# Optimization experiments

Measured on AMD Instinct MI355X. Metric: run time of the kernel, lower is better.

The kernel has to match this reference:

```python
import jax, jax.numpy as jnp
import numpy as np

D = 8        # q_ndim (= dof_ndim)
HID = 200    # hidden_size
N = 16384    # batch of states
EPS = 0.1    # qdot regularizer coefficient in L()


def _lagrangian(z, Ws, bs):
    # z: (2D,) = [q, qdot]; angular_dims=() so CosSin is an identity pass-through
    v = z[D:]
    h = z
    for W, b in zip(Ws[:-1], bs[:-1]):
        h = jax.nn.softplus(h @ W + b)   # FCsoftplus blocks
    L = (h @ Ws[-1] + bs[-1])[0]          # final Linear -> scalar (Reshape(-1))
    return L + EPS * jnp.dot(v, v)


def setup_inputs():
    key = jax.random.key(0)
    ks = jax.random.split(key, 5)
    z = jax.random.normal(ks[0], (N, 2 * D), dtype=jnp.float32)
    t = jnp.zeros((), dtype=jnp.float32)

    def lin(k, fi, fo, scale):
        return (jax.random.normal(k, (fi, fo), dtype=jnp.float32)
                * jnp.float32(scale / np.sqrt(fi)))

    W0 = lin(ks[1], 2 * D, HID, 1.0)
    W1 = lin(ks[2], HID, HID, 1.0)
    W2 = lin(ks[3], HID, HID, 1.0)
    W3 = lin(ks[4], HID, 1, 0.01)  # small head keeps mass matrix M well conditioned
    b0 = jnp.zeros((HID,), jnp.float32)  # zero_bias init per FCsoftplus/Linear
    b1 = jnp.zeros((HID,), jnp.float32)
    b2 = jnp.zeros((HID,), jnp.float32)
    b3 = jnp.zeros((1,), jnp.float32)
    return dict(t=t, z=z, W0=W0, b0=b0, W1=W1, b1=b1, W2=W2, b2=b2, W3=W3, b3=b3)


def reference(t, z, W0, b0, W1, b1, W2, b2, W3, b3):
    # Euler-Lagrange dynamics (LagrangianDynamics):
    #   M a = dL/dq - (d2L/dq dv) v,  M = d2L/dv2;  dz/dt = [v, a]
    Ws = (W0, W1, W2, W3)
    bs = (b0, b1, b2, b3)
    Lfn = lambda zz: _lagrangian(zz, Ws, bs)

    def dyn_single(zi):
        g = jax.grad(Lfn)(zi)              # (2D,)  = [dL/dq, dL/dv]
        H = jax.jacfwd(jax.grad(Lfn))(zi)  # (2D,2D) Hessian of L wrt z
        v = zi[D:]
        M = H[D:, D:]                      # d(dL/dv)/dv  -> mass matrix
        C = H[D:, :D]                      # d(dL/dv)/dq
        F = g[:D] - C @ v
        a = jnp.linalg.solve(M, F)
        return jnp.concatenate([v, a])     # (2D,)

    return jax.vmap(dyn_single)(z)         # (N, 2D)
```

## Files before the change

kernel.cpp:

```cpp
#include <hip/hip_runtime.h>
#include <math.h>

#define DD 8
#define ZD 16
#define HID 200
#define EPSL 0.1f
#define BS 16
#define NTHREADS 1024
#define NKC 7
#define NMT 13
#define XSTR 216
#define CSTR 216
#define WSTR 208
#define HSTR 20
#define NT4 4

#define KSC 1024.0f
#define SSC 64.0f
#define INV_K (1.0f/1024.0f)
#define INV_KS (1.0f/65536.0f)

typedef _Float16 half8 __attribute__((ext_vector_type(8)));
typedef _Float16 half4v __attribute__((ext_vector_type(4)));
typedef _Float16 half2v __attribute__((ext_vector_type(2)));
typedef float float4v __attribute__((ext_vector_type(4)));

#define S4 (NKC*NMT*64*8)
#define OFF_W1T 0
#define OFF_W2T (S4)
#define OFF_W1  (2*S4)
#define OFF_W2  (3*S4)
#define OFF_W0T (4*S4)
#define OFF_W0  (4*S4 + NMT*64*8)
#define WS_HALFS (4*S4 + NMT*64*8 + NKC*64*8)

#define CFSZ  (16*CSTR)
#define O_XT  0
#define O_XB  (128*XSTR + 8)
#define O_CF  (O_XB + 128*XSTR)
#define O_BSH (O_CF + 5*CFSZ)
#define O_W0T (O_BSH + 4*WSTR)
#define O_XZ  (O_W0T + 8*WSTR + 24)
#define O_GSH (O_XZ + 16*40)
#define O_HR  (O_GSH + 256)
#define SMEM_HALFS (O_HR + 128*HSTR*2)

__global__ void prep(const float* __restrict__ W0, const float* __restrict__ W1,
                     const float* __restrict__ W2, _Float16* __restrict__ ws)
{
    int idx = blockIdx.x * 256 + threadIdx.x;
    if (idx >= WS_HALFS) return;
    float v = 0.f;
    if (idx < 4*S4) {
        int arr = idx / S4, e = idx % S4;
        int kc = e / (NMT*64*8); int r = e % (NMT*64*8);
        int mt = r / (64*8); r %= 64*8;
        int lane = r / 8, j = r % 8;
        int m = mt*16 + (lane & 15);
        int k = kc*32 + (lane >> 4)*8 + j;
        if (m < HID && k < HID) {
            if      (arr == 0) v = W1[k*HID + m];
            else if (arr == 1) v = W2[k*HID + m];
            else if (arr == 2) v = W1[m*HID + k];
            else               v = W2[m*HID + k];
        }
    } else if (idx < OFF_W0) {
        int e = idx - OFF_W0T;
        int mt = e / (64*8); int r = e % (64*8);
        int lane = r / 8, j = r % 8;
        int m = mt*16 + (lane & 15);
        int k = (lane >> 4)*8 + j;
        if (m < HID && k < ZD) v = W0[k*HID + m];
    } else {
        int e = idx - OFF_W0;
        int kc = e / (64*8); int r = e % (64*8);
        int lane = r / 8, j = r % 8;
        int m = (lane & 15);
        int k = kc*32 + (lane >> 4)*8 + j;
        if (k < HID) v = W0[m*HID + k];
    }
    ws[idx] = (_Float16)v;
}

__device__ __forceinline__ half4v pk4(float4v a) {
    half2v lo = __builtin_bit_cast(half2v, __builtin_amdgcn_cvt_pkrtz(a.x, a.y));
    half2v hi = __builtin_bit_cast(half2v, __builtin_amdgcn_cvt_pkrtz(a.z, a.w));
    return __builtin_shufflevector(lo, hi, 0, 1, 2, 3);
}
__device__ __forceinline__ void sig_sp(float x, float& sp, float& sg) {
    float e = __expf(-fabsf(x));
    float r = 1.0f / (1.0f + e);
    sg = (x >= 0.f) ? r : (1.0f - r);
    sp = fmaxf(x, 0.f) + __logf(1.f + e);
}

template<int NTILES>
__device__ __forceinline__ void run_mv(const half8* __restrict__ Asw,
                                       const _Float16* __restrict__ Xsrc,
                                       int mt0, int mtc, int lane,
                                       float4v acc[2][NTILES])
{
    const int lm = lane & 15, q = lane >> 4;
#pragma unroll
    for (int m = 0; m < 2; ++m)
#pragma unroll
        for (int n = 0; n < NTILES; ++n)
            acc[m][n] = (float4v){0.f, 0.f, 0.f, 0.f};
    for (int kc = 0; kc < NKC; ++kc) {
        half8 a[2];
#pragma unroll
        for (int m = 0; m < 2; ++m)
            if (m < mtc) a[m] = Asw[(kc*NMT + mt0 + m)*64 + lane];
        half8 x[NTILES];
#pragma unroll
        for (int n = 0; n < NTILES; ++n)
            x[n] = *(const half8*)(Xsrc + (n*16 + lm)*XSTR + kc*32 + q*8);
#pragma unroll
        for (int m = 0; m < 2; ++m)
            if (m < mtc)
#pragma unroll
                for (int n = 0; n < NTILES; ++n)
                    acc[m][n] = __builtin_amdgcn_mfma_f32_16x16x32_f16(a[m], x[n], acc[m][n], 0, 0, 0);
    }
}

__global__ void __launch_bounds__(NTHREADS, 4)
lnn_main(const float* __restrict__ z,
         const float* __restrict__ W0, const float* __restrict__ b0,
         const float* __restrict__ b1, const float* __restrict__ b2,
         const float* __restrict__ W3,
         const _Float16* __restrict__ ws,
         float* __restrict__ out)
{
    __shared__ alignas(16) _Float16 smem[SMEM_HALFS];
    _Float16* const Xt  = smem + O_XT;
    _Float16* const Xb  = smem + O_XB;
    _Float16* const Cf  = smem + O_CF;
    _Float16* const bsh = smem + O_BSH;
    _Float16* const w0t = smem + O_W0T;
    _Float16* const Xz  = smem + O_XZ;
    float*    const gsh = (float*)(smem + O_GSH);
    float*    const Hr  = (float*)(smem + O_HR);
    _Float16* const FB  = smem + O_HR;

    const int tid  = threadIdx.x;
    const int wave = tid >> 6;
    const int lane = tid & 63;
    const int lm   = lane & 15;
    const int q    = lane >> 4;
    const int s0   = blockIdx.x * BS;

    const int twm  = wave >> 1;
    const int twn  = wave & 1;
    const int mt0t = (twm < 5) ? twm*2 : (twm + 5);
    const int mtct = (twm < 5) ? 2 : 1;

    const half8* W1Tsw = (const half8*)(ws + OFF_W1T);
    const half8* W2Tsw = (const half8*)(ws + OFF_W2T);
    const half8* W1sw  = (const half8*)(ws + OFF_W1);
    const half8* W2sw  = (const half8*)(ws + OFF_W2);
    const half8* W0Tsw = (const half8*)(ws + OFF_W0T);
    const half8* W0sw  = (const half8*)(ws + OFF_W0);

    if (tid < 256) {
        int s = tid >> 4, k = tid & 15;
        Xz[s*40 + k]      = (_Float16)z[(s0 + s)*ZD + k];
        Xz[s*40 + 16 + k] = (_Float16)0.f;
    }
    for (int idx = tid; idx < 128*16; idx += NTHREADS) {
        int r = idx >> 4, c = 200 + (idx & 15);
        Xt[r*XSTR + c] = (_Float16)0.f;
        Xb[r*XSTR + c] = (_Float16)0.f;
    }
    for (int idx = tid; idx < 16*16; idx += NTHREADS) {
        int r = idx >> 4, c = 200 + (idx & 15);
        FB[r*XSTR + c] = (_Float16)0.f;
    }
    if (tid < 8) {
        Xt[128*XSTR + tid] = (_Float16)0.f;
        FB[16*XSTR + tid]  = (_Float16)0.f;
    }
    for (int idx = tid; idx < 5*16*8; idx += NTHREADS) {
        int j = idx >> 7, r = (idx >> 3) & 15, c = 208 + (idx & 7);
        Cf[j*CFSZ + r*CSTR + c] = (_Float16)0.f;
    }
    for (int idx = tid; idx < 4*WSTR; idx += NTHREADS) {
        int l = idx / WSTR, u = idx % WSTR;
        float v = 0.f;
        if (u < HID) {
            if      (l == 0) v = b0[u];
            else if (l == 1) v = b1[u];
            else if (l == 2) v = b2[u];
            else             v = KSC * W3[u];
        }
        bsh[idx] = (_Float16)v;
    }
    for (int idx = tid; idx < 8*WSTR + 24; idx += NTHREADS) {
        int t = idx / WSTR, u = idx % WSTR;
        w0t[idx] = (_Float16)((t < 8 && u < HID) ? SSC * W0[(DD + t)*HID + u] : 0.f);
    }
    __syncthreads();

    float4v acc1[2][1];
    float4v acc4[2][NT4];
    const int ubf = wave*16 + q*4;

    if (wave < NMT) {
        acc1[0][0] = (float4v){0.f,0.f,0.f,0.f};
        half8 xz = *(const half8*)(Xz + lm*40 + q*8);
        half8 aw = W0Tsw[wave*64 + lane];
        acc1[0][0] = __builtin_amdgcn_mfma_f32_16x16x32_f16(aw, xz, acc1[0][0], 0, 0, 0);
        half4v bb = *(const half4v*)(&bsh[0*WSTR + ubf]);
        float h[4], p[4];
#pragma unroll
        for (int r = 0; r < 4; ++r) {
            float av = acc1[0][0][r] + (float)bb[r];
            sig_sp(av, h[r], p[r]);
        }
        *(half4v*)(&FB[lm*XSTR + ubf])          = pk4((float4v){h[0],h[1],h[2],h[3]});
        *(half4v*)(&Cf[0*CFSZ + lm*CSTR + ubf]) = pk4((float4v){p[0],p[1],p[2],p[3]});
    }
    __syncthreads();

    if (wave < NMT) run_mv<1>(W1Tsw, FB, wave, 1, lane, acc1);
    __syncthreads();
    if (wave < NMT) {
        half4v bb = *(const half4v*)(&bsh[1*WSTR + ubf]);
        float h[4], p[4];
#pragma unroll
        for (int r = 0; r < 4; ++r) {
            float av = acc1[0][0][r] + (float)bb[r];
            sig_sp(av, h[r], p[r]);
        }
        *(half4v*)(&FB[lm*XSTR + ubf])          = pk4((float4v){h[0],h[1],h[2],h[3]});
        *(half4v*)(&Cf[1*CFSZ + lm*CSTR + ubf]) = pk4((float4v){p[0],p[1],p[2],p[3]});
    }
    __syncthreads();

    {
#pragma unroll
        for (int m = 0; m < 2; ++m)
#pragma unroll
            for (int n = 0; n < NT4; ++n)
                acc4[m][n] = (float4v){0.f, 0.f, 0.f, 0.f};
        for (int kc = 0; kc < NKC; ++kc) {
            half8 a[2];
#pragma unroll
            for (int m = 0; m < 2; ++m)
                if (m < mtct) a[m] = W1Tsw[(kc*NMT + mt0t + m)*64 + lane];
            half8 p0 = *(const half8*)(Cf + 0*CFSZ + lm*CSTR + kc*32 + q*8);
            half8 x[NT4];
#pragma unroll
            for (int n = 0; n < NT4; ++n) {
                half8 w0 = *(const half8*)(w0t + (twn*NT4 + n)*WSTR + kc*32 + q*8);
                x[n] = p0 * w0;
            }
#pragma unroll
            for (int m = 0; m < 2; ++m)
                if (m < mtct)
#pragma unroll
                    for (int n = 0; n < NT4; ++n)
                        acc4[m][n] = __builtin_amdgcn_mfma_f32_16x16x32_f16(a[m], x[n], acc4[m][n], 0, 0, 0);
        }
        if (wave < NMT) run_mv<1>(W2Tsw, FB, wave, 1, lane, acc1);
    }
    __syncthreads();
#pragma unroll
    for (int m = 0; m < 2; ++m)
        if (m < mtct) {
            const int ub = (mt0t + m)*16 + q*4;
            half4v p1 = *(const half4v*)(&Cf[1*CFSZ + lm*CSTR + ub]);
#pragma unroll
            for (int n = 0; n < NT4; ++n) {
                int row = (twn*NT4 + n)*16 + lm;
                *(half4v*)(&Xt[row*XSTR + ub]) = pk4(acc4[m][n]) * p1;
            }
        }
    if (wave < NMT) {
        half4v bb = *(const half4v*)(&bsh[2*WSTR + ubf]);
        half4v w3 = *(const half4v*)(&bsh[3*WSTR + ubf]);
        float d2[4], c2[4];
#pragma unroll
        for (int r = 0; r < 4; ++r) {
            float av = acc1[0][0][r] + (float)bb[r];
            float e = __expf(-fabsf(av));
            float rr = 1.f / (1.f + e);
            float sg = (av >= 0.f) ? rr : (1.f - rr);
            float wk = (float)w3[r];
            d2[r] = wk * sg;
            c2[r] = wk * sg * (1.f - sg);
        }
        *(half4v*)(&FB[lm*XSTR + ubf])          = pk4((float4v){d2[0],d2[1],d2[2],d2[3]});
        *(half4v*)(&Cf[2*CFSZ + lm*CSTR + ubf]) = pk4((float4v){c2[0],c2[1],c2[2],c2[3]});
    }
    __syncthreads();

    run_mv<NT4>(W2Tsw, Xt + twn*64*XSTR, mt0t, mtct, lane, acc4);
    if (wave < NMT) run_mv<1>(W2sw, FB, wave, 1, lane, acc1);
    __syncthreads();
#pragma unroll
    for (int m = 0; m < 2; ++m)
        if (m < mtct) {
            const int ub = (mt0t + m)*16 + q*4;
            half4v c2 = *(const half4v*)(&Cf[2*CFSZ + lm*CSTR + ub]);
#pragma unroll
            for (int n = 0; n < NT4; ++n) {
                int row = (twn*NT4 + n)*16 + lm;
                *(half4v*)(&Xb[row*XSTR + ub]) = pk4(acc4[m][n]) * c2;
            }
        }
    if (wave < NMT) {
        half4v p1 = *(const half4v*)(&Cf[1*CFSZ + lm*CSTR + ubf]);
        half4v u1 = pk4(acc1[0][0]);
        half4v one = {(_Float16)1.f,(_Float16)1.f,(_Float16)1.f,(_Float16)1.f};
        *(half4v*)(&FB[lm*XSTR + ubf])          = u1 * p1;
        *(half4v*)(&Cf[3*CFSZ + lm*CSTR + ubf]) = u1 * (one - p1);
    }
    __syncthreads();

    run_mv<NT4>(W2sw, Xb + twn*64*XSTR, mt0t, mtct, lane, acc4);
    if (wave < NMT) run_mv<1>(W1sw, FB, wave, 1, lane, acc1);
    __syncthreads();
#pragma unroll
    for (int m = 0; m < 2; ++m)
        if (m < mtct) {
            const int ub = (mt0t + m)*16 + q*4;
            half4v p1 = *(const half4v*)(&Cf[1*CFSZ + lm*CSTR + ub]);
            half4v c3 = *(const half4v*)(&Cf[3*CFSZ + lm*CSTR + ub]);
#pragma unroll
            for (int n = 0; n < NT4; ++n) {
                int row = (twn*NT4 + n)*16 + lm;
                half4v th1 = *(const half4v*)(&Xt[row*XSTR + ub]);
                *(half4v*)(&Xb[row*XSTR + ub]) = pk4(acc4[m][n]) * p1 + c3 * th1;
            }
        }
    if (wave < NMT) {
        half4v p0 = *(const half4v*)(&Cf[0*CFSZ + lm*CSTR + ubf]);
        half4v u0 = pk4(acc1[0][0]);
        half4v one = {(_Float16)1.f,(_Float16)1.f,(_Float16)1.f,(_Float16)1.f};
        half4v d0 = u0 * p0;
        *(half4v*)(&FB[lm*XSTR + ubf])          = d0;
        *(half4v*)(&Cf[4*CFSZ + lm*CSTR + ubf]) = d0 * (one - p0);
    }
    __syncthreads();

    run_mv<NT4>(W1sw, Xb + twn*64*XSTR, mt0t, mtct, lane, acc4);
    if (wave == 13) {
        float4v g = (float4v){0.f,0.f,0.f,0.f};
        for (int kc = 0; kc < NKC; ++kc) {
            half8 a = W0sw[kc*64 + lane];
            half8 x = *(const half8*)(FB + lm*XSTR + kc*32 + q*8);
            g = __builtin_amdgcn_mfma_f32_16x16x32_f16(a, x, g, 0, 0, 0);
        }
        if (q < 2) {
            float4v gv;
            gv.x = g.x*INV_K; gv.y = g.y*INV_K; gv.z = g.z*INV_K; gv.w = g.w*INV_K;
            *(float4v*)(&gsh[lm*8 + q*4]) = gv;
        }
    }
#pragma unroll
    for (int m = 0; m < 2; ++m)
        if (m < mtct) {
            const int ub = (mt0t + m)*16 + q*4;
            half4v p0 = *(const half4v*)(&Cf[0*CFSZ + lm*CSTR + ub]);
            half4v c4 = *(const half4v*)(&Cf[4*CFSZ + lm*CSTR + ub]);
#pragma unroll
            for (int n = 0; n < NT4; ++n) {
                int row = (twn*NT4 + n)*16 + lm;
                half4v w0 = *(const half4v*)(&w0t[(twn*NT4 + n)*WSTR + ub]);
                *(half4v*)(&Xt[row*XSTR + ub]) = pk4(acc4[m][n]) * p0 + c4 * w0;
            }
        }
    __syncthreads();

    if (wave < 8) {
        float4v hacc = (float4v){0.f,0.f,0.f,0.f};
        for (int kc = 0; kc < NKC; ++kc) {
            half8 a = W0sw[kc*64 + lane];
            half8 x = *(const half8*)(Xt + (wave*16 + lm)*XSTR + kc*32 + q*8);
            hacc = __builtin_amdgcn_mfma_f32_16x16x32_f16(a, x, hacc, 0, 0, 0);
        }
        int row = wave*16 + lm;
        float4v hv;
        hv.x = hacc.x*INV_KS; hv.y = hacc.y*INV_KS;
        hv.z = hacc.z*INV_KS; hv.w = hacc.w*INV_KS;
        *(float4v*)(&Hr[row*HSTR + q*4]) = hv;
    }
    __syncthreads();

    if (tid < BS) {
        const int s = tid;
        float M[DD][DD], F[DD], v[DD], a[DD];
#pragma unroll
        for (int c = 0; c < DD; ++c) v[c] = z[(s0 + s)*ZD + DD + c];
#pragma unroll
        for (int r = 0; r < DD; ++r) {
            float f = gsh[s*8 + r];
#pragma unroll
            for (int c = 0; c < DD; ++c) {
                M[r][c] = Hr[(r*16 + s)*HSTR + DD + c] + ((r == c) ? 2.f*EPSL : 0.f);
                f -= Hr[(r*16 + s)*HSTR + c] * v[c];
            }
            F[r] = f;
        }
#pragma unroll
        for (int col = 0; col < DD; ++col) {
            const float inv = 1.f / M[col][col];
#pragma unroll
            for (int r = col + 1; r < DD; ++r) {
                const float fac = M[r][col] * inv;
#pragma unroll
                for (int c = col + 1; c < DD; ++c) M[r][c] -= fac * M[col][c];
                F[r] -= fac * F[col];
            }
        }
#pragma unroll
        for (int r = DD - 1; r >= 0; --r) {
            float ssum = F[r];
#pragma unroll
            for (int c = r + 1; c < DD; ++c) ssum -= M[r][c] * a[c];
            a[r] = ssum / M[r][r];
        }
        float* op = out + (size_t)(s0 + s)*ZD;
#pragma unroll
        for (int c = 0; c < DD; ++c) { op[c] = v[c]; op[DD + c] = a[c]; }
    }
}

extern "C" void kernel_launch(void* const* d_in, const int* in_sizes, int n_in,
                              void* d_out, int out_size, void* d_ws, size_t ws_size,
                              hipStream_t stream)
{
    const float* z  = (const float*)d_in[1];
    const float* W0 = (const float*)d_in[2];
    const float* b0 = (const float*)d_in[3];
    const float* W1 = (const float*)d_in[4];
    const float* b1 = (const float*)d_in[5];
    const float* W2 = (const float*)d_in[6];
    const float* b2 = (const float*)d_in[7];
    const float* W3 = (const float*)d_in[8];
    float* out = (float*)d_out;
    _Float16* ws = (_Float16*)d_ws;

    const int n = in_sizes[1] / (2*DD);

    prep<<<dim3((WS_HALFS + 255)/256), dim3(256), 0, stream>>>(W0, W1, W2, ws);
    lnn_main<<<dim3(n / BS), dim3(NTHREADS), 0, stream>>>(
        z, W0, b0, b1, b2, W3, ws, out);
}
```

Baseline: 156.6 us.

## Halve samples per block to shrink LDS and raise occupancy

Reduces the per-block batch from 16 to 8 states, so the tangent matrices hold 64 rows instead of 128 and LDS buffers shrink; launch bounds now request 8 blocks per CU. Indexing of per-sample coefficients is remapped (sq/tq) so each 16-row MFMA tile covers 8 samples by 2 tangent directions. The 16-wide first-layer and gradient MFMAs now waste half their columns, and weight fragments are reloaded for twice as many blocks, trading redundant work and weight traffic for higher occupancy and better latency hiding. Some padding and zeroing logic is also removed.

```diff
diff --git a/kernel.cpp b/kernel.cpp
--- a/kernel.cpp
+++ b/kernel.cpp
@@ -5,15 +5,16 @@
 #define ZD 16
 #define HID 200
 #define EPSL 0.1f
-#define BS 16
+#define BS 8
 #define NTHREADS 1024
 #define NKC 7
 #define NMT 13
 #define XSTR 216
-#define CSTR 216
-#define WSTR 208
-#define HSTR 20
-#define NT4 4
+#define CSTR 208
+#define BSTR 200
+#define W0STR 200
+#define HSTR 16
+#define NT4 2
 
 #define KSC 1024.0f
 #define SSC 64.0f
@@ -34,16 +35,16 @@
 #define OFF_W0  (4*S4 + NMT*64*8)
 #define WS_HALFS (4*S4 + NMT*64*8 + NKC*64*8)
 
-#define CFSZ  (16*CSTR)
+#define CFSZ  (8*CSTR)
 #define O_XT  0
-#define O_XB  (128*XSTR + 8)
-#define O_CF  (O_XB + 128*XSTR)
-#define O_BSH (O_CF + 5*CFSZ)
-#define O_W0T (O_BSH + 4*WSTR)
-#define O_XZ  (O_W0T + 8*WSTR + 24)
-#define O_GSH (O_XZ + 16*40)
-#define O_HR  (O_GSH + 256)
-#define SMEM_HALFS (O_HR + 128*HSTR*2)
+#define O_XB  (O_XT + 64*XSTR + 8)
+#define O_CF  (O_XB + 64*XSTR)
+#define O_U   (O_CF + 5*CFSZ)
+#define O_XZ  (O_U + 2048)
+#define O_GSH (O_XZ + 320)
+#define O_BSH (O_GSH + 128)
+#define O_W0T (O_BSH + 4*BSTR)
+#define SMEM_HALFS (O_W0T + 8*W0STR + 24)
 
 __global__ void prep(const float* __restrict__ W0, const float* __restrict__ W1,
                      const float* __restrict__ W2, _Float16* __restrict__ ws)
@@ -124,7 +125,7 @@
     }
 }
 
-__global__ void __launch_bounds__(NTHREADS, 4)
+__global__ void __launch_bounds__(NTHREADS, 8)
 lnn_main(const float* __restrict__ z,
          const float* __restrict__ W0, const float* __restrict__ b0,
          const float* __restrict__ b1, const float* __restrict__ b2,
@@ -140,14 +141,16 @@
     _Float16* const w0t = smem + O_W0T;
     _Float16* const Xz  = smem + O_XZ;
     float*    const gsh = (float*)(smem + O_GSH);
-    float*    const Hr  = (float*)(smem + O_HR);
-    _Float16* const FB  = smem + O_HR;
+    float*    const Hr  = (float*)(smem + O_U);
+    _Float16* const FB  = smem + O_U;
 
     const int tid  = threadIdx.x;
     const int wave = tid >> 6;
     const int lane = tid & 63;
     const int lm   = lane & 15;
     const int q    = lane >> 4;
+    const int sq   = lane & 7;
+    const int tq   = (lane >> 3) & 1;
     const int s0   = blockIdx.x * BS;
 
     const int twm  = wave >> 1;
@@ -162,42 +165,36 @@
     const half8* W0Tsw = (const half8*)(ws + OFF_W0T);
     const half8* W0sw  = (const half8*)(ws + OFF_W0);
 
-    if (tid < 256) {
+    if (tid < 128) {
         int s = tid >> 4, k = tid & 15;
         Xz[s*40 + k]      = (_Float16)z[(s0 + s)*ZD + k];
         Xz[s*40 + 16 + k] = (_Float16)0.f;
     }
-    for (int idx = tid; idx < 128*16; idx += NTHREADS) {
+    for (int idx = tid; idx < 64*16; idx += NTHREADS) {
         int r = idx >> 4, c = 200 + (idx & 15);
         Xt[r*XSTR + c] = (_Float16)0.f;
         Xb[r*XSTR + c] = (_Float16)0.f;
     }
-    for (int idx = tid; idx < 16*16; idx += NTHREADS) {
+    for (int idx = tid; idx < 8*16; idx += NTHREADS) {
         int r = idx >> 4, c = 200 + (idx & 15);
         FB[r*XSTR + c] = (_Float16)0.f;
     }
     if (tid < 8) {
-        Xt[128*XSTR + tid] = (_Float16)0.f;
-        FB[16*XSTR + tid]  = (_Float16)0.f;
-    }
-    for (int idx = tid; idx < 5*16*8; idx += NTHREADS) {
-        int j = idx >> 7, r = (idx >> 3) & 15, c = 208 + (idx & 7);
-        Cf[j*CFSZ + r*CSTR + c] = (_Float16)0.f;
-    }
-    for (int idx = tid; idx < 4*WSTR; idx += NTHREADS) {
-        int l = idx / WSTR, u = idx % WSTR;
-        float v = 0.f;
-        if (u < HID) {
-            if      (l == 0) v = b0[u];
-            else if (l == 1) v = b1[u];
-            else if (l == 2) v = b2[u];
-            else             v = KSC * W3[u];
-        }
+        Xt[64*XSTR + tid] = (_Float16)0.f;
+        FB[8*XSTR + tid]  = (_Float16)0.f;
+    }
+    for (int idx = tid; idx < 4*BSTR; idx += NTHREADS) {
+        int l = idx / BSTR, u = idx % BSTR;
+        float v;
+        if      (l == 0) v = b0[u];
+        else if (l == 1) v = b1[u];
+        else if (l == 2) v = b2[u];
+        else             v = KSC * W3[u];
         bsh[idx] = (_Float16)v;
     }
-    for (int idx = tid; idx < 8*WSTR + 24; idx += NTHREADS) {
-        int t = idx / WSTR, u = idx % WSTR;
-        w0t[idx] = (_Float16)((t < 8 && u < HID) ? SSC * W0[(DD + t)*HID + u] : 0.f);
+    for (int idx = tid; idx < 8*W0STR + 24; idx += NTHREADS) {
+        int t = idx / W0STR, u = idx % W0STR;
+        w0t[idx] = (_Float16)((t < 8) ? SSC * W0[(DD + t)*HID + u] : 0.f);
     }
     __syncthreads();
 
@@ -210,22 +207,24 @@
         half8 xz = *(const half8*)(Xz + lm*40 + q*8);
         half8 aw = W0Tsw[wave*64 + lane];
         acc1[0][0] = __builtin_amdgcn_mfma_f32_16x16x32_f16(aw, xz, acc1[0][0], 0, 0, 0);
-        half4v bb = *(const half4v*)(&bsh[0*WSTR + ubf]);
-        float h[4], p[4];
-#pragma unroll
-        for (int r = 0; r < 4; ++r) {
-            float av = acc1[0][0][r] + (float)bb[r];
-            sig_sp(av, h[r], p[r]);
-        }
-        *(half4v*)(&FB[lm*XSTR + ubf])          = pk4((float4v){h[0],h[1],h[2],h[3]});
-        *(half4v*)(&Cf[0*CFSZ + lm*CSTR + ubf]) = pk4((float4v){p[0],p[1],p[2],p[3]});
+        if (lm < 8) {
+            half4v bb = *(const half4v*)(&bsh[0*BSTR + ubf]);
+            float h[4], p[4];
+#pragma unroll
+            for (int r = 0; r < 4; ++r) {
+                float av = acc1[0][0][r] + (float)bb[r];
+                sig_sp(av, h[r], p[r]);
+            }
+            *(half4v*)(&FB[lm*XSTR + ubf])        = pk4((float4v){h[0],h[1],h[2],h[3]});
+            *(half4v*)(&Cf[0*CFSZ + lm*CSTR + ubf]) = pk4((float4v){p[0],p[1],p[2],p[3]});
+        }
     }
     __syncthreads();
 
     if (wave < NMT) run_mv<1>(W1Tsw, FB, wave, 1, lane, acc1);
     __syncthreads();
-    if (wave < NMT) {
-        half4v bb = *(const half4v*)(&bsh[1*WSTR + ubf]);
+    if (wave < NMT && lm < 8) {
+        half4v bb = *(const half4v*)(&bsh[1*BSTR + ubf]);
         float h[4], p[4];
 #pragma unroll
         for (int r = 0; r < 4; ++r) {
@@ -248,11 +247,12 @@
 #pragma unroll
             for (int m = 0; m < 2; ++m)
                 if (m < mtct) a[m] = W1Tsw[(kc*NMT + mt0t + m)*64 + lane];
-            half8 p0 = *(const half8*)(Cf + 0*CFSZ + lm*CSTR + kc*32 + q*8);
+            half8 p0 = *(const half8*)(Cf + 0*CFSZ + sq*CSTR + kc*32 + q*8);
             half8 x[NT4];
 #pragma unroll
             for (int n = 0; n < NT4; ++n) {
-                half8 w0 = *(const half8*)(w0t + (twn*NT4 + n)*WSTR + kc*32 + q*8);
+                int t = 2*(twn*NT4 + n) + tq;
+                half8 w0 = *(const half8*)(w0t + t*W0STR + kc*32 + q*8);
                 x[n] = p0 * w0;
             }
 #pragma unroll
@@ -269,16 +269,16 @@
     for (int m = 0; m < 2; ++m)
         if (m < mtct) {
             const int ub = (mt0t + m)*16 + q*4;
-            half4v p1 = *(const half4v*)(&Cf[1*CFSZ + lm*CSTR + ub]);
+            half4v p1 = *(const half4v*)(&Cf[1*CFSZ + sq*CSTR + ub]);
 #pragma unroll
             for (int n = 0; n < NT4; ++n) {
                 int row = (twn*NT4 + n)*16 + lm;
                 *(half4v*)(&Xt[row*XSTR + ub]) = pk4(acc4[m][n]) * p1;
             }
         }
-    if (wave < NMT) {
-        half4v bb = *(const half4v*)(&bsh[2*WSTR + ubf]);
-        half4v w3 = *(const half4v*)(&bsh[3*WSTR + ubf]);
+    if (wave < NMT && lm < 8) {
+        half4v bb = *(const half4v*)(&bsh[2*BSTR + ubf]);
+        half4v w3 = *(const half4v*)(&bsh[3*BSTR + ubf]);
         float d2[4], c2[4];
 #pragma unroll
         for (int r = 0; r < 4; ++r) {
@@ -295,21 +295,21 @@
     }
     __syncthreads();
 
-    run_mv<NT4>(W2Tsw, Xt + twn*64*XSTR, mt0t, mtct, lane, acc4);
+    run_mv<NT4>(W2Tsw, Xt + twn*32*XSTR, mt0t, mtct, lane, acc4);
     if (wave < NMT) run_mv<1>(W2sw, FB, wave, 1, lane, acc1);
     __syncthreads();
 #pragma unroll
     for (int m = 0; m < 2; ++m)
         if (m < mtct) {
             const int ub = (mt0t + m)*16 + q*4;
-            half4v c2 = *(const half4v*)(&Cf[2*CFSZ + lm*CSTR + ub]);
+            half4v c2 = *(const half4v*)(&Cf[2*CFSZ + sq*CSTR + ub]);
 #pragma unroll
             for (int n = 0; n < NT4; ++n) {
                 int row = (twn*NT4 + n)*16 + lm;
                 *(half4v*)(&Xb[row*XSTR + ub]) = pk4(acc4[m][n]) * c2;
             }
         }
-    if (wave < NMT) {
+    if (wave < NMT && lm < 8) {
         half4v p1 = *(const half4v*)(&Cf[1*CFSZ + lm*CSTR + ubf]);
         half4v u1 = pk4(acc1[0][0]);
         half4v one = {(_Float16)1.f,(_Float16)1.f,(_Float16)1.f,(_Float16)1.f};
@@ -318,15 +318,15 @@
     }
     __syncthreads();
 
-    run_mv<NT4>(W2sw, Xb + twn*64*XSTR, mt0t, mtct, lane, acc4);
+    run_mv<NT4>(W2sw, Xb + twn*32*XSTR, mt0t, mtct, lane, acc4);
     if (wave < NMT) run_mv<1>(W1sw, FB, wave, 1, lane, acc1);
     __syncthreads();
 #pragma unroll
     for (int m = 0; m < 2; ++m)
         if (m < mtct) {
             const int ub = (mt0t + m)*16 + q*4;
-            half4v p1 = *(const half4v*)(&Cf[1*CFSZ + lm*CSTR + ub]);
-            half4v c3 = *(const half4v*)(&Cf[3*CFSZ + lm*CSTR + ub]);
+            half4v p1 = *(const half4v*)(&Cf[1*CFSZ + sq*CSTR + ub]);
+            half4v c3 = *(const half4v*)(&Cf[3*CFSZ + sq*CSTR + ub]);
 #pragma unroll
             for (int n = 0; n < NT4; ++n) {
                 int row = (twn*NT4 + n)*16 + lm;
@@ -334,7 +334,7 @@
                 *(half4v*)(&Xb[row*XSTR + ub]) = pk4(acc4[m][n]) * p1 + c3 * th1;
             }
         }
-    if (wave < NMT) {
+    if (wave < NMT && lm < 8) {
         half4v p0 = *(const half4v*)(&Cf[0*CFSZ + lm*CSTR + ubf]);
         half4v u0 = pk4(acc1[0][0]);
         half4v one = {(_Float16)1.f,(_Float16)1.f,(_Float16)1.f,(_Float16)1.f};
@@ -344,7 +344,7 @@
     }
     __syncthreads();
 
-    run_mv<NT4>(W1sw, Xb + twn*64*XSTR, mt0t, mtct, lane, acc4);
+    run_mv<NT4>(W1sw, Xb + twn*32*XSTR, mt0t, mtct, lane, acc4);
     if (wave == 13) {
         float4v g = (float4v){0.f,0.f,0.f,0.f};
         for (int kc = 0; kc < NKC; ++kc) {
@@ -352,7 +352,7 @@
             half8 x = *(const half8*)(FB + lm*XSTR + kc*32 + q*8);
             g = __builtin_amdgcn_mfma_f32_16x16x32_f16(a, x, g, 0, 0, 0);
         }
-        if (q < 2) {
+        if (q < 2 && lm < 8) {
             float4v gv;
             gv.x = g.x*INV_K; gv.y = g.y*INV_K; gv.z = g.z*INV_K; gv.w = g.w*INV_K;
             *(float4v*)(&gsh[lm*8 + q*4]) = gv;
@@ -362,18 +362,19 @@
     for (int m = 0; m < 2; ++m)
         if (m < mtct) {
             const int ub = (mt0t + m)*16 + q*4;
-            half4v p0 = *(const half4v*)(&Cf[0*CFSZ + lm*CSTR + ub]);
-            half4v c4 = *(const half4v*)(&Cf[4*CFSZ + lm*CSTR + ub]);
+            half4v p0 = *(const half4v*)(&Cf[0*CFSZ + sq*CSTR + ub]);
+            half4v c4 = *(const half4v*)(&Cf[4*CFSZ + sq*CSTR + ub]);
 #pragma unroll
             for (int n = 0; n < NT4; ++n) {
                 int row = (twn*NT4 + n)*16 + lm;
-                half4v w0 = *(const half4v*)(&w0t[(twn*NT4 + n)*WSTR + ub]);
+                int t = 2*(twn*NT4 + n) + tq;
+                half4v w0 = *(const half4v*)(&w0t[t*W0STR + ub]);
                 *(half4v*)(&Xt[row*XSTR + ub]) = pk4(acc4[m][n]) * p0 + c4 * w0;
             }
         }
     __syncthreads();
 
-    if (wave < 8) {
+    if (wave < 4) {
         float4v hacc = (float4v){0.f,0.f,0.f,0.f};
         for (int kc = 0; kc < NKC; ++kc) {
             half8 a = W0sw[kc*64 + lane];
@@ -398,8 +399,8 @@
             float f = gsh[s*8 + r];
 #pragma unroll
             for (int c = 0; c < DD; ++c) {
-                M[r][c] = Hr[(r*16 + s)*HSTR + DD + c] + ((r == c) ? 2.f*EPSL : 0.f);
-                f -= Hr[(r*16 + s)*HSTR + c] * v[c];
+                M[r][c] = Hr[(r*8 + s)*HSTR + DD + c] + ((r == c) ? 2.f*EPSL : 0.f);
+                f -= Hr[(r*8 + s)*HSTR + c] * v[c];
             }
             F[r] = f;
         }
```

Measured after the change: 240.6 us. +53.6%, slower.

## Remap wave tiling to 4 M-tiles by 2 N-tiles per wave

Applied to the files above, without the earlier changes.

Changes the per-wave MFMA tile assignment for the tangent matvecs from 2 M-tiles by 4 N-tiles (two N groups) to 4 M-tiles by 2 N-tiles (four N groups). Each wave now loads more weight fragments and fewer activation fragments per k-chunk, which shifts the LDS/global load mix and the load balance across the 16 waves. The last M group holds only one tile, so its waves do far less work than the others, which risks a more imbalanced schedule.

```diff
diff --git a/kernel.cpp b/kernel.cpp
--- a/kernel.cpp
+++ b/kernel.cpp
@@ -13,7 +13,7 @@
 #define CSTR 216
 #define WSTR 208
 #define HSTR 20
-#define NT4 4
+#define NT4 2
 
 #define KSC 1024.0f
 #define SSC 64.0f
@@ -94,32 +94,32 @@
     sp = fmaxf(x, 0.f) + __logf(1.f + e);
 }
 
-template<int NTILES>
+template<int MT, int NT>
 __device__ __forceinline__ void run_mv(const half8* __restrict__ Asw,
                                        const _Float16* __restrict__ Xsrc,
                                        int mt0, int mtc, int lane,
-                                       float4v acc[2][NTILES])
+                                       float4v acc[MT][NT])
 {
     const int lm = lane & 15, q = lane >> 4;
 #pragma unroll
-    for (int m = 0; m < 2; ++m)
-#pragma unroll
-        for (int n = 0; n < NTILES; ++n)
+    for (int m = 0; m < MT; ++m)
+#pragma unroll
+        for (int n = 0; n < NT; ++n)
             acc[m][n] = (float4v){0.f, 0.f, 0.f, 0.f};
     for (int kc = 0; kc < NKC; ++kc) {
-        half8 a[2];
-#pragma unroll
-        for (int m = 0; m < 2; ++m)
+        half8 a[MT];
+#pragma unroll
+        for (int m = 0; m < MT; ++m)
             if (m < mtc) a[m] = Asw[(kc*NMT + mt0 + m)*64 + lane];
-        half8 x[NTILES];
-#pragma unroll
-        for (int n = 0; n < NTILES; ++n)
+        half8 x[NT];
+#pragma unroll
+        for (int n = 0; n < NT; ++n)
             x[n] = *(const half8*)(Xsrc + (n*16 + lm)*XSTR + kc*32 + q*8);
 #pragma unroll
-        for (int m = 0; m < 2; ++m)
+        for (int m = 0; m < MT; ++m)
             if (m < mtc)
 #pragma unroll
-                for (int n = 0; n < NTILES; ++n)
+                for (int n = 0; n < NT; ++n)
                     acc[m][n] = __builtin_amdgcn_mfma_f32_16x16x32_f16(a[m], x[n], acc[m][n], 0, 0, 0);
     }
 }
@@ -150,10 +150,10 @@
     const int q    = lane >> 4;
     const int s0   = blockIdx.x * BS;
 
-    const int twm  = wave >> 1;
-    const int twn  = wave & 1;
-    const int mt0t = (twm < 5) ? twm*2 : (twm + 5);
-    const int mtct = (twm < 5) ? 2 : 1;
+    const int ng   = wave & 3;
+    const int mg   = wave >> 2;
+    const int mt0t = mg * 4;
+    const int mtct = (mg < 3) ? 4 : 1;
 
     const half8* W1Tsw = (const half8*)(ws + OFF_W1T);
     const half8* W2Tsw = (const half8*)(ws + OFF_W2T);
@@ -201,8 +201,8 @@
     }
     __syncthreads();
 
-    float4v acc1[2][1];
-    float4v acc4[2][NT4];
+    float4v acc1[1][1];
+    float4v acc4[4][NT4];
     const int ubf = wave*16 + q*4;
 
     if (wave < NMT) {
@@ -222,7 +222,7 @@
     }
     __syncthreads();
 
-    if (wave < NMT) run_mv<1>(W1Tsw, FB, wave, 1, lane, acc1);
+    if (wave < NMT) run_mv<1,1>(W1Tsw, FB, wave, 1, lane, acc1);
     __syncthreads();
     if (wave < NMT) {
         half4v bb = *(const half4v*)(&bsh[1*WSTR + ubf]);
@@ -239,40 +239,40 @@
 
     {
 #pragma unroll
-        for (int m = 0; m < 2; ++m)
+        for (int m = 0; m < 4; ++m)
 #pragma unroll
             for (int n = 0; n < NT4; ++n)
                 acc4[m][n] = (float4v){0.f, 0.f, 0.f, 0.f};
         for (int kc = 0; kc < NKC; ++kc) {
-            half8 a[2];
-#pragma unroll
-            for (int m = 0; m < 2; ++m)
+            half8 a[4];
+#pragma unroll
+            for (int m = 0; m < 4; ++m)
                 if (m < mtct) a[m] = W1Tsw[(kc*NMT + mt0t + m)*64 + lane];
             half8 p0 = *(const half8*)(Cf + 0*CFSZ + lm*CSTR + kc*32 + q*8);
             half8 x[NT4];
 #pragma unroll
             for (int n = 0; n < NT4; ++n) {
-                half8 w0 = *(const half8*)(w0t + (twn*NT4 + n)*WSTR + kc*32 + q*8);
+                half8 w0 = *(const half8*)(w0t + (ng*NT4 + n)*WSTR + kc*32 + q*8);
                 x[n] = p0 * w0;
             }
 #pragma unroll
-            for (int m = 0; m < 2; ++m)
+            for (int m = 0; m < 4; ++m)
                 if (m < mtct)
 #pragma unroll
                     for (int n = 0; n < NT4; ++n)
                         acc4[m][n] = __builtin_amdgcn_mfma_f32_16x16x32_f16(a[m], x[n], acc4[m][n], 0, 0, 0);
         }
-        if (wave < NMT) run_mv<1>(W2Tsw, FB, wave, 1, lane, acc1);
-    }
-    __syncthreads();
-#pragma unroll
-    for (int m = 0; m < 2; ++m)
+        if (wave < NMT) run_mv<1,1>(W2Tsw, FB, wave, 1, lane, acc1);
+    }
+    __syncthreads();
+#pragma unroll
+    for (int m = 0; m < 4; ++m)
         if (m < mtct) {
             const int ub = (mt0t + m)*16 + q*4;
             half4v p1 = *(const half4v*)(&Cf[1*CFSZ + lm*CSTR + ub]);
 #pragma unroll
             for (int n = 0; n < NT4; ++n) {
-                int row = (twn*NT4 + n)*16 + lm;
+                int row = (ng*NT4 + n)*16 + lm;
                 *(half4v*)(&Xt[row*XSTR + ub]) = pk4(acc4[m][n]) * p1;
             }
         }
@@ -295,17 +295,17 @@
     }
     __syncthreads();
 
-    run_mv<NT4>(W2Tsw, Xt + twn*64*XSTR, mt0t, mtct, lane, acc4);
-    if (wave < NMT) run_mv<1>(W2sw, FB, wave, 1, lane, acc1);
-    __syncthreads();
-#pragma unroll
-    for (int m = 0; m < 2; ++m)
+    run_mv<4,NT4>(W2Tsw, Xt + ng*32*XSTR, mt0t, mtct, lane, acc4);
+    if (wave < NMT) run_mv<1,1>(W2sw, FB, wave, 1, lane, acc1);
+    __syncthreads();
+#pragma unroll
+    for (int m = 0; m < 4; ++m)
         if (m < mtct) {
             const int ub = (mt0t + m)*16 + q*4;
             half4v c2 = *(const half4v*)(&Cf[2*CFSZ + lm*CSTR + ub]);
 #pragma unroll
             for (int n = 0; n < NT4; ++n) {
-                int row = (twn*NT4 + n)*16 + lm;
+                int row = (ng*NT4 + n)*16 + lm;
                 *(half4v*)(&Xb[row*XSTR + ub]) = pk4(acc4[m][n]) * c2;
             }
         }
@@ -318,18 +318,18 @@
     }
     __syncthreads();
 
-    run_mv<NT4>(W2sw, Xb + twn*64*XSTR, mt0t, mtct, lane, acc4);
-    if (wave < NMT) run_mv<1>(W1sw, FB, wave, 1, lane, acc1);
-    __syncthreads();
-#pragma unroll
-    for (int m = 0; m < 2; ++m)
+    run_mv<4,NT4>(W2sw, Xb + ng*32*XSTR, mt0t, mtct, lane, acc4);
+    if (wave < NMT) run_mv<1,1>(W1sw, FB, wave, 1, lane, acc1);
+    __syncthreads();
+#pragma unroll
+    for (int m = 0; m < 4; ++m)
         if (m < mtct) {
             const int ub = (mt0t + m)*16 + q*4;
             half4v p1 = *(const half4v*)(&Cf[1*CFSZ + lm*CSTR + ub]);
             half4v c3 = *(const half4v*)(&Cf[3*CFSZ + lm*CSTR + ub]);
 #pragma unroll
             for (int n = 0; n < NT4; ++n) {
-                int row = (twn*NT4 + n)*16 + lm;
+                int row = (ng*NT4 + n)*16 + lm;
                 half4v th1 = *(const half4v*)(&Xt[row*XSTR + ub]);
                 *(half4v*)(&Xb[row*XSTR + ub]) = pk4(acc4[m][n]) * p1 + c3 * th1;
             }
@@ -344,7 +344,7 @@
     }
     __syncthreads();
 
-    run_mv<NT4>(W1sw, Xb + twn*64*XSTR, mt0t, mtct, lane, acc4);
+    run_mv<4,NT4>(W1sw, Xb + ng*32*XSTR, mt0t, mtct, lane, acc4);
     if (wave == 13) {
         float4v g = (float4v){0.f,0.f,0.f,0.f};
         for (int kc = 0; kc < NKC; ++kc) {
@@ -359,15 +359,15 @@
         }
     }
 #pragma unroll
-    for (int m = 0; m < 2; ++m)
+    for (int m = 0; m < 4; ++m)
         if (m < mtct) {
             const int ub = (mt0t + m)*16 + q*4;
             half4v p0 = *(const half4v*)(&Cf[0*CFSZ + lm*CSTR + ub]);
             half4v c4 = *(const half4v*)(&Cf[4*CFSZ + lm*CSTR + ub]);
 #pragma unroll
             for (int n = 0; n < NT4; ++n) {
-                int row = (twn*NT4 + n)*16 + lm;
-                half4v w0 = *(const half4v*)(&w0t[(twn*NT4 + n)*WSTR + ub]);
+                int row = (ng*NT4 + n)*16 + lm;
+                half4v w0 = *(const half4v*)(&w0t[(ng*NT4 + n)*WSTR + ub]);
                 *(half4v*)(&Xt[row*XSTR + ub]) = pk4(acc4[m][n]) * p0 + c4 * w0;
             }
         }
```

New measurement: 166.8 us. +6.5%, slower.

## Pipeline forward and tangent passes to cut block barriers, double-buffer feedback rows

Applied to the files above, without the earlier changes.

Restructures the per-block schedule so the scalar (forward/backward) matvec chain and the 128-row tangent matmuls run in the same phase. Double-buffered FB arrays replace the single one, so several __syncthreads can be removed. Elementwise sigmoid/coefficient scaling is folded into the operand loads of the next MFMA pass (run_mv_mod and the final W0 pass) instead of separate write-back passes. The z load is done directly into registers, and the LDS footprint shrinks by aliasing Hr onto Xb. The trade-off is extra per-k-chunk vector multiplies and some risk around reuse and padding of the aliased buffers.

```diff
diff --git a/kernel.cpp b/kernel.cpp
--- a/kernel.cpp
+++ b/kernel.cpp
@@ -10,7 +10,8 @@
 #define NKC 7
 #define NMT 13
 #define XSTR 216
-#define CSTR 216
+#define CSTR 208
+#define FBSTR 200
 #define WSTR 208
 #define HSTR 20
 #define NT4 4
@@ -37,13 +38,13 @@
 #define CFSZ  (16*CSTR)
 #define O_XT  0
 #define O_XB  (128*XSTR + 8)
-#define O_CF  (O_XB + 128*XSTR)
-#define O_BSH (O_CF + 5*CFSZ)
+#define O_CF  (O_XB + 128*XSTR + 8)
+#define O_FBA (O_CF + 5*CFSZ)
+#define O_FBB (O_FBA + 16*FBSTR + 24)
+#define O_BSH (O_FBB + 16*FBSTR + 24)
 #define O_W0T (O_BSH + 4*WSTR)
-#define O_XZ  (O_W0T + 8*WSTR + 24)
-#define O_GSH (O_XZ + 16*40)
-#define O_HR  (O_GSH + 256)
-#define SMEM_HALFS (O_HR + 128*HSTR*2)
+#define O_GSH (O_W0T + 8*WSTR + 24)
+#define SMEM_HALFS (O_GSH + 256)
 
 __global__ void prep(const float* __restrict__ W0, const float* __restrict__ W1,
                      const float* __restrict__ W2, _Float16* __restrict__ ws)
@@ -94,32 +95,66 @@
     sp = fmaxf(x, 0.f) + __logf(1.f + e);
 }
 
-template<int NTILES>
+template<int MT, int NT, int STR>
 __device__ __forceinline__ void run_mv(const half8* __restrict__ Asw,
                                        const _Float16* __restrict__ Xsrc,
                                        int mt0, int mtc, int lane,
-                                       float4v acc[2][NTILES])
+                                       float4v acc[MT][NT])
 {
     const int lm = lane & 15, q = lane >> 4;
 #pragma unroll
+    for (int m = 0; m < MT; ++m)
+#pragma unroll
+        for (int n = 0; n < NT; ++n)
+            acc[m][n] = (float4v){0.f, 0.f, 0.f, 0.f};
+    for (int kc = 0; kc < NKC; ++kc) {
+        half8 a[MT];
+#pragma unroll
+        for (int m = 0; m < MT; ++m)
+            if (m < mtc) a[m] = Asw[(kc*NMT + mt0 + m)*64 + lane];
+        half8 x[NT];
+#pragma unroll
+        for (int n = 0; n < NT; ++n)
+            x[n] = *(const half8*)(Xsrc + (n*16 + lm)*STR + kc*32 + q*8);
+#pragma unroll
+        for (int m = 0; m < MT; ++m)
+            if (m < mtc)
+#pragma unroll
+                for (int n = 0; n < NT; ++n)
+                    acc[m][n] = __builtin_amdgcn_mfma_f32_16x16x32_f16(a[m], x[n], acc[m][n], 0, 0, 0);
+    }
+}
+
+template<int NT>
+__device__ __forceinline__ void run_mv_mod(const half8* __restrict__ Asw,
+                                           const _Float16* __restrict__ Xsrc,
+                                           const _Float16* __restrict__ crow,
+                                           int mt0, int mtc, int lane,
+                                           float4v acc[2][NT])
+{
+    const int lm = lane & 15, q = lane >> 4;
+#pragma unroll
     for (int m = 0; m < 2; ++m)
 #pragma unroll
-        for (int n = 0; n < NTILES; ++n)
+        for (int n = 0; n < NT; ++n)
             acc[m][n] = (float4v){0.f, 0.f, 0.f, 0.f};
     for (int kc = 0; kc < NKC; ++kc) {
         half8 a[2];
 #pragma unroll
         for (int m = 0; m < 2; ++m)
             if (m < mtc) a[m] = Asw[(kc*NMT + mt0 + m)*64 + lane];
-        half8 x[NTILES];
-#pragma unroll
-        for (int n = 0; n < NTILES; ++n)
-            x[n] = *(const half8*)(Xsrc + (n*16 + lm)*XSTR + kc*32 + q*8);
+        half8 cm = *(const half8*)(crow + kc*32 + q*8);
+        half8 x[NT];
+#pragma unroll
+        for (int n = 0; n < NT; ++n) {
+            half8 xv = *(const half8*)(Xsrc + (n*16 + lm)*XSTR + kc*32 + q*8);
+            x[n] = xv * cm;
+        }
 #pragma unroll
         for (int m = 0; m < 2; ++m)
             if (m < mtc)
 #pragma unroll
-                for (int n = 0; n < NTILES; ++n)
+                for (int n = 0; n < NT; ++n)
                     acc[m][n] = __builtin_amdgcn_mfma_f32_16x16x32_f16(a[m], x[n], acc[m][n], 0, 0, 0);
     }
 }
@@ -136,12 +171,12 @@
     _Float16* const Xt  = smem + O_XT;
     _Float16* const Xb  = smem + O_XB;
     _Float16* const Cf  = smem + O_CF;
+    _Float16* const FBa = smem + O_FBA;
+    _Float16* const FBb = smem + O_FBB;
     _Float16* const bsh = smem + O_BSH;
     _Float16* const w0t = smem + O_W0T;
-    _Float16* const Xz  = smem + O_XZ;
     float*    const gsh = (float*)(smem + O_GSH);
-    float*    const Hr  = (float*)(smem + O_HR);
-    _Float16* const FB  = smem + O_HR;
+    float*    const Hr  = (float*)(smem + O_XB);
 
     const int tid  = threadIdx.x;
     const int wave = tid >> 6;
@@ -162,27 +197,30 @@
     const half8* W0Tsw = (const half8*)(ws + OFF_W0T);
     const half8* W0sw  = (const half8*)(ws + OFF_W0);
 
-    if (tid < 256) {
-        int s = tid >> 4, k = tid & 15;
-        Xz[s*40 + k]      = (_Float16)z[(s0 + s)*ZD + k];
-        Xz[s*40 + 16 + k] = (_Float16)0.f;
-    }
+    const int ubf = wave*16 + q*4;
+    const half4v one = {(_Float16)1.f,(_Float16)1.f,(_Float16)1.f,(_Float16)1.f};
+
+    float4v acc1[1][1];
+    float4v acc4[2][NT4];
+
     for (int idx = tid; idx < 128*16; idx += NTHREADS) {
         int r = idx >> 4, c = 200 + (idx & 15);
         Xt[r*XSTR + c] = (_Float16)0.f;
         Xb[r*XSTR + c] = (_Float16)0.f;
     }
-    for (int idx = tid; idx < 16*16; idx += NTHREADS) {
-        int r = idx >> 4, c = 200 + (idx & 15);
-        FB[r*XSTR + c] = (_Float16)0.f;
-    }
     if (tid < 8) {
         Xt[128*XSTR + tid] = (_Float16)0.f;
-        FB[16*XSTR + tid]  = (_Float16)0.f;
-    }
-    for (int idx = tid; idx < 5*16*8; idx += NTHREADS) {
-        int j = idx >> 7, r = (idx >> 3) & 15, c = 208 + (idx & 7);
-        Cf[j*CFSZ + r*CSTR + c] = (_Float16)0.f;
+        Xb[128*XSTR + tid] = (_Float16)0.f;
+    }
+    if (tid >= 32 && tid < 80) {
+        int t = tid - 32;
+        if (t < 24) FBa[16*FBSTR + t] = (_Float16)0.f;
+        else        FBb[16*FBSTR + (t-24)] = (_Float16)0.f;
+    }
+    if (tid >= 128 && tid < 176) {
+        int t = tid - 128;
+        int j = 1 + t/16, c = t & 15;
+        Cf[j*CFSZ + c] = (_Float16)0.f;
     }
     for (int idx = tid; idx < 4*WSTR; idx += NTHREADS) {
         int l = idx / WSTR, u = idx % WSTR;
@@ -199,44 +237,32 @@
         int t = idx / WSTR, u = idx % WSTR;
         w0t[idx] = (_Float16)((t < 8 && u < HID) ? SSC * W0[(DD + t)*HID + u] : 0.f);
     }
-    __syncthreads();
-
-    float4v acc1[2][1];
-    float4v acc4[2][NT4];
-    const int ubf = wave*16 + q*4;
 
     if (wave < NMT) {
+        half8 xz;
+#pragma unroll
+        for (int j = 0; j < 8; ++j) xz[j] = (_Float16)0.f;
+        if (q < 2) {
+            const float* zp = z + (size_t)(s0 + lm)*ZD + q*8;
+#pragma unroll
+            for (int j = 0; j < 8; ++j) xz[j] = (_Float16)zp[j];
+        }
         acc1[0][0] = (float4v){0.f,0.f,0.f,0.f};
-        half8 xz = *(const half8*)(Xz + lm*40 + q*8);
         half8 aw = W0Tsw[wave*64 + lane];
         acc1[0][0] = __builtin_amdgcn_mfma_f32_16x16x32_f16(aw, xz, acc1[0][0], 0, 0, 0);
-        half4v bb = *(const half4v*)(&bsh[0*WSTR + ubf]);
         float h[4], p[4];
 #pragma unroll
         for (int r = 0; r < 4; ++r) {
-            float av = acc1[0][0][r] + (float)bb[r];
+            float bb = (ubf < HID) ? b0[ubf + r] : 0.f;
+            float av = acc1[0][0][r] + bb;
             sig_sp(av, h[r], p[r]);
         }
-        *(half4v*)(&FB[lm*XSTR + ubf])          = pk4((float4v){h[0],h[1],h[2],h[3]});
+        if (ubf < 200) *(half4v*)(&FBa[lm*FBSTR + ubf]) = pk4((float4v){h[0],h[1],h[2],h[3]});
         *(half4v*)(&Cf[0*CFSZ + lm*CSTR + ubf]) = pk4((float4v){p[0],p[1],p[2],p[3]});
     }
     __syncthreads();
 
-    if (wave < NMT) run_mv<1>(W1Tsw, FB, wave, 1, lane, acc1);
-    __syncthreads();
-    if (wave < NMT) {
-        half4v bb = *(const half4v*)(&bsh[1*WSTR + ubf]);
-        float h[4], p[4];
-#pragma unroll
-        for (int r = 0; r < 4; ++r) {
-            float av = acc1[0][0][r] + (float)bb[r];
-            sig_sp(av, h[r], p[r]);
-        }
-        *(half4v*)(&FB[lm*XSTR + ubf])          = pk4((float4v){h[0],h[1],h[2],h[3]});
-        *(half4v*)(&Cf[1*CFSZ + lm*CSTR + ubf]) = pk4((float4v){p[0],p[1],p[2],p[3]});
-    }
-    __syncthreads();
-
+    if (wave < NMT) run_mv<1,1,FBSTR>(W1Tsw, FBa, wave, 1, lane, acc1);
     {
 #pragma unroll
         for (int m = 0; m < 2; ++m)
@@ -262,18 +288,40 @@
                     for (int n = 0; n < NT4; ++n)
                         acc4[m][n] = __builtin_amdgcn_mfma_f32_16x16x32_f16(a[m], x[n], acc4[m][n], 0, 0, 0);
         }
-        if (wave < NMT) run_mv<1>(W2Tsw, FB, wave, 1, lane, acc1);
-    }
-    __syncthreads();
+    }
 #pragma unroll
     for (int m = 0; m < 2; ++m)
         if (m < mtct) {
             const int ub = (mt0t + m)*16 + q*4;
-            half4v p1 = *(const half4v*)(&Cf[1*CFSZ + lm*CSTR + ub]);
 #pragma unroll
             for (int n = 0; n < NT4; ++n) {
-                int row = (twn*NT4 + n)*16 + lm;
-                *(half4v*)(&Xt[row*XSTR + ub]) = pk4(acc4[m][n]) * p1;
+                int row = twn*64 + n*16 + lm;
+                *(half4v*)(&Xt[row*XSTR + ub]) = pk4(acc4[m][n]);
+            }
+        }
+    if (wave < NMT) {
+        half4v bb = *(const half4v*)(&bsh[1*WSTR + ubf]);
+        float h[4], p[4];
+#pragma unroll
+        for (int r = 0; r < 4; ++r) {
+            float av = acc1[0][0][r] + (float)bb[r];
+            sig_sp(av, h[r], p[r]);
+        }
+        if (ubf < 200) *(half4v*)(&FBb[lm*FBSTR + ubf]) = pk4((float4v){h[0],h[1],h[2],h[3]});
+        *(half4v*)(&Cf[1*CFSZ + lm*CSTR + ubf]) = pk4((float4v){p[0],p[1],p[2],p[3]});
+    }
+    __syncthreads();
+
+    if (wave < NMT) run_mv<1,1,FBSTR>(W2Tsw, FBb, wave, 1, lane, acc1);
+    run_mv_mod<NT4>(W2Tsw, Xt + twn*64*XSTR, Cf + 1*CFSZ + lm*CSTR, mt0t, mtct, lane, acc4);
+#pragma unroll
+    for (int m = 0; m < 2; ++m)
+        if (m < mtct) {
+            const int ub = (mt0t + m)*16 + q*4;
+#pragma unroll
+            for (int n = 0; n < NT4; ++n) {
+                int row = twn*64 + n*16 + lm;
+                *(half4v*)(&Xb[row*XSTR + ub]) = pk4(acc4[m][n]);
             }
         }
     if (wave < NMT) {
@@ -290,36 +338,19 @@
             d2[r] = wk * sg;
             c2[r] = wk * sg * (1.f - sg);
         }
-        *(half4v*)(&FB[lm*XSTR + ubf])          = pk4((float4v){d2[0],d2[1],d2[2],d2[3]});
+        if (ubf < 200) *(half4v*)(&FBa[lm*FBSTR + ubf]) = pk4((float4v){d2[0],d2[1],d2[2],d2[3]});
         *(half4v*)(&Cf[2*CFSZ + lm*CSTR + ubf]) = pk4((float4v){c2[0],c2[1],c2[2],c2[3]});
     }
     __syncthreads();
 
-    run_mv<NT4>(W2Tsw, Xt + twn*64*XSTR, mt0t, mtct, lane, acc4);
-    if (wave < NMT) run_mv<1>(W2sw, FB, wave, 1, lane, acc1);
-    __syncthreads();
-#pragma unroll
-    for (int m = 0; m < 2; ++m)
-        if (m < mtct) {
-            const int ub = (mt0t + m)*16 + q*4;
-            half4v c2 = *(const half4v*)(&Cf[2*CFSZ + lm*CSTR + ub]);
-#pragma unroll
-            for (int n = 0; n < NT4; ++n) {
-                int row = (twn*NT4 + n)*16 + lm;
-                *(half4v*)(&Xb[row*XSTR + ub]) = pk4(acc4[m][n]) * c2;
-            }
-        }
+    if (wave < NMT) run_mv<1,1,FBSTR>(W2sw, FBa, wave, 1, lane, acc1);
+    run_mv_mod<NT4>(W2sw, Xb + twn*64*XSTR, Cf + 2*CFSZ + lm*CSTR, mt0t, mtct, lane, acc4);
     if (wave < NMT) {
         half4v p1 = *(const half4v*)(&Cf[1*CFSZ + lm*CSTR + ubf]);
         half4v u1 = pk4(acc1[0][0]);
-        half4v one = {(_Float16)1.f,(_Float16)1.f,(_Float16)1.f,(_Float16)1.f};
-        *(half4v*)(&FB[lm*XSTR + ubf])          = u1 * p1;
+        if (ubf < 200) *(half4v*)(&FBb[lm*FBSTR + ubf]) = u1 * p1;
         *(half4v*)(&Cf[3*CFSZ + lm*CSTR + ubf]) = u1 * (one - p1);
     }
-    __syncthreads();
-
-    run_mv<NT4>(W2sw, Xb + twn*64*XSTR, mt0t, mtct, lane, acc4);
-    if (wave < NMT) run_mv<1>(W1sw, FB, wave, 1, lane, acc1);
     __syncthreads();
 #pragma unroll
     for (int m = 0; m < 2; ++m)
@@ -329,55 +360,43 @@
             half4v c3 = *(const half4v*)(&Cf[3*CFSZ + lm*CSTR + ub]);
 #pragma unroll
             for (int n = 0; n < NT4; ++n) {
-                int row = (twn*NT4 + n)*16 + lm;
-                half4v th1 = *(const half4v*)(&Xt[row*XSTR + ub]);
-                *(half4v*)(&Xb[row*XSTR + ub]) = pk4(acc4[m][n]) * p1 + c3 * th1;
+                int row = twn*64 + n*16 + lm;
+                half4v xt = *(const half4v*)(&Xt[row*XSTR + ub]);
+                *(half4v*)(&Xb[row*XSTR + ub]) = pk4(acc4[m][n]) * p1 + c3 * (xt * p1);
+            }
+        }
+    __syncthreads();
+
+    if (wave < NMT) run_mv<1,1,FBSTR>(W1sw, FBb, wave, 1, lane, acc1);
+    run_mv<2,NT4,XSTR>(W1sw, Xb + twn*64*XSTR, mt0t, mtct, lane, acc4);
+#pragma unroll
+    for (int m = 0; m < 2; ++m)
+        if (m < mtct) {
+            const int ub = (mt0t + m)*16 + q*4;
+#pragma unroll
+            for (int n = 0; n < NT4; ++n) {
+                int row = twn*64 + n*16 + lm;
+                *(half4v*)(&Xt[row*XSTR + ub]) = pk4(acc4[m][n]);
             }
         }
     if (wave < NMT) {
         half4v p0 = *(const half4v*)(&Cf[0*CFSZ + lm*CSTR + ubf]);
         half4v u0 = pk4(acc1[0][0]);
-        half4v one = {(_Float16)1.f,(_Float16)1.f,(_Float16)1.f,(_Float16)1.f};
         half4v d0 = u0 * p0;
-        *(half4v*)(&FB[lm*XSTR + ubf])          = d0;
+        if (ubf < 200) *(half4v*)(&FBa[lm*FBSTR + ubf]) = d0;
         *(half4v*)(&Cf[4*CFSZ + lm*CSTR + ubf]) = d0 * (one - p0);
     }
-    __syncthreads();
-
-    run_mv<NT4>(W1sw, Xb + twn*64*XSTR, mt0t, mtct, lane, acc4);
-    if (wave == 13) {
-        float4v g = (float4v){0.f,0.f,0.f,0.f};
-        for (int kc = 0; kc < NKC; ++kc) {
-            half8 a = W0sw[kc*64 + lane];
-            half8 x = *(const half8*)(FB + lm*XSTR + kc*32 + q*8);
-            g = __builtin_amdgcn_mfma_f32_16x16x32_f16(a, x, g, 0, 0, 0);
-        }
-        if (q < 2) {
-            float4v gv;
-            gv.x = g.x*INV_K; gv.y = g.y*INV_K; gv.z = g.z*INV_K; gv.w = g.w*INV_K;
-            *(float4v*)(&gsh[lm*8 + q*4]) = gv;
-        }
-    }
-#pragma unroll
-    for (int m = 0; m < 2; ++m)
-        if (m < mtct) {
-            const int ub = (mt0t + m)*16 + q*4;
-            half4v p0 = *(const half4v*)(&Cf[0*CFSZ + lm*CSTR + ub]);
-            half4v c4 = *(const half4v*)(&Cf[4*CFSZ + lm*CSTR + ub]);
-#pragma unroll
-            for (int n = 0; n < NT4; ++n) {
-                int row = (twn*NT4 + n)*16 + lm;
-                half4v w0 = *(const half4v*)(&w0t[(twn*NT4 + n)*WSTR + ub]);
-                *(half4v*)(&Xt[row*XSTR + ub]) = pk4(acc4[m][n]) * p0 + c4 * w0;
-            }
-        }
     __syncthreads();
 
     if (wave < 8) {
         float4v hacc = (float4v){0.f,0.f,0.f,0.f};
         for (int kc = 0; kc < NKC; ++kc) {
-            half8 a = W0sw[kc*64 + lane];
-            half8 x = *(const half8*)(Xt + (wave*16 + lm)*XSTR + kc*32 + q*8);
+            half8 a  = W0sw[kc*64 + lane];
+            half8 xt = *(const half8*)(Xt + (wave*16 + lm)*XSTR + kc*32 + q*8);
+            half8 p0 = *(const half8*)(Cf + 0*CFSZ + lm*CSTR + kc*32 + q*8);
+            half8 c4 = *(const half8*)(Cf + 4*CFSZ + lm*CSTR + kc*32 + q*8);
+            half8 w0 = *(const half8*)(w0t + wave*WSTR + kc*32 + q*8);
+            half8 x  = xt * p0 + c4 * w0;
             hacc = __builtin_amdgcn_mfma_f32_16x16x32_f16(a, x, hacc, 0, 0, 0);
         }
         int row = wave*16 + lm;
@@ -385,6 +404,18 @@
         hv.x = hacc.x*INV_KS; hv.y = hacc.y*INV_KS;
         hv.z = hacc.z*INV_KS; hv.w = hacc.w*INV_KS;
         *(float4v*)(&Hr[row*HSTR + q*4]) = hv;
+    } else if (wave == 8) {
+        float4v g = (float4v){0.f,0.f,0.f,0.f};
+        for (int kc = 0; kc < NKC; ++kc) {
+            half8 a = W0sw[kc*64 + lane];
+            half8 x = *(const half8*)(FBa + lm*FBSTR + kc*32 + q*8);
+            g = __builtin_amdgcn_mfma_f32_16x16x32_f16(a, x, g, 0, 0, 0);
+        }
+        if (q < 2) {
+            float4v gv;
+            gv.x = g.x*INV_K; gv.y = g.y*INV_K; gv.z = g.z*INV_K; gv.w = g.w*INV_K;
+            *(float4v*)(&gsh[lm*8 + q*4]) = gv;
+        }
     }
     __syncthreads();
 
```

After: 157.5 us. No clear change (+0.6%).
